# Optimization experiments

Measured on AMD Instinct MI355X. Metric: run time of the kernel, lower is better.

## Reference

```python
import jax, jax.numpy as jnp
import numpy as np

N_FEATURES = 16384
N_EXPERTS = 8
D_IN = 768
EXPERT_DIM = N_FEATURES // N_EXPERTS  # 2048
N_TOKENS = 16384


def setup_inputs() -> dict:
    key = jax.random.key(0)
    k_act, k_preb, k_enc, k_dec, k_rb, k_r = jax.random.split(key, 6)
    activations = jax.random.normal(k_act, (N_TOKENS, D_IN), dtype=jnp.float32)
    pre_b = jax.random.normal(k_preb, (D_IN,), dtype=jnp.float32) * 0.01
    enc = jax.random.normal(k_enc, (N_EXPERTS, D_IN, EXPERT_DIM), dtype=jnp.float32) / (2.0 ** 0.5) / (D_IN ** 0.5)
    dec = jax.random.normal(k_dec, (N_EXPERTS, EXPERT_DIM, D_IN), dtype=jnp.float32) / (EXPERT_DIM ** 0.5)
    router_b = jax.random.normal(k_rb, (D_IN,), dtype=jnp.float32) * 0.01
    router = jax.random.normal(k_r, (D_IN, N_EXPERTS), dtype=jnp.float32) / (D_IN ** 0.5)
    return {"activations": activations, "pre_b": pre_b, "enc": enc, "dec": dec,
            "router_b": router_b, "router": router}


def reference(activations, pre_b, enc, dec, router_b, router):
    # Router: softmax over experts, top-1 routing.
    logits = (activations - router_b) @ router            # [N, E]
    probs = jax.nn.softmax(logits, axis=-1)
    expert_max_prob = jnp.max(probs, axis=-1)              # [N]
    expert_idx = jnp.argmax(probs, axis=-1)                # [N] int

    n_experts = enc.shape[0]
    recons = jnp.zeros_like(activations)
    # Fixed small loop over experts; tokens are masked (zeroed) per expert so
    # each per-expert encode/decode GEMM only contributes for its routed rows.
    for e in range(n_experts):
        mask = (expert_idx == e)[:, None]                  # [N, 1]
        x_e = jnp.where(mask, activations, 0.0)            # masked gather
        latent = jax.nn.relu(x_e @ enc[e])                 # [N, expert_dim]
        recon = latent @ dec[e]                            # [N, d_in]
        recons = recons + jnp.where(mask, recon, 0.0)      # scatter-combine

    return expert_max_prob[:, None] * recons + pre_b
```

## Files before the change

kernel.cpp:

```cpp
#include <hip/hip_runtime.h>
#include <hip/hip_bf16.h>
#include <hip/hip_fp16.h>

#define N_TOKENS 16384
#define D_IN 768
#define N_EXPERTS 8
#define EXPERT_DIM 2048

#define ROUTER_BLOCKS 256
#define TOK_PER_BLOCK 64

typedef _Float16 half8 __attribute__((ext_vector_type(8)));
typedef float floatx4 __attribute__((ext_vector_type(4)));

#define BM 128
#define BN 128
#define BK 32

#define WAIT_VM4 0xF74
#define WAIT_VM0 0xF70

__device__ __forceinline__ void glds16(const _Float16* g, _Float16* l) {
    __builtin_amdgcn_global_load_lds(
        (const __attribute__((address_space(1))) unsigned int*)g,
        (__attribute__((address_space(3))) unsigned int*)l, 16, 0, 0);
}

__global__ __launch_bounds__(256) void convert_act(const float* __restrict__ act,
    _Float16* __restrict__ act_h)
{
    size_t i = ((size_t)blockIdx.x * 256 + threadIdx.x) * 8;
    float4 v0 = *(const float4*)(act + i);
    float4 v1 = *(const float4*)(act + i + 4);
    half8 h;
    h[0] = (_Float16)v0.x; h[1] = (_Float16)v0.y; h[2] = (_Float16)v0.z; h[3] = (_Float16)v0.w;
    h[4] = (_Float16)v1.x; h[5] = (_Float16)v1.y; h[6] = (_Float16)v1.z; h[7] = (_Float16)v1.w;
    *(half8*)(act_h + i) = h;
}

__global__ __launch_bounds__(256) void router_kernel(const float* __restrict__ act,
    const float* __restrict__ router_b, const float* __restrict__ router,
    float* __restrict__ prob, int* __restrict__ localpos, int* __restrict__ eidx,
    int* __restrict__ hist)
{
    __shared__ int h[N_EXPERTS];
    if (threadIdx.x < N_EXPERTS) h[threadIdx.x] = 0;
    __syncthreads();

    int wave = threadIdx.x >> 6, lane = threadIdx.x & 63;
#pragma unroll 1
    for (int it = 0; it < 16; ++it) {
        int t = blockIdx.x * TOK_PER_BLOCK + wave * 16 + it;
        float acc[8];
#pragma unroll
        for (int e = 0; e < 8; ++e) acc[e] = 0.f;
        const float* arow = act + (size_t)t * D_IN;
#pragma unroll
        for (int i0 = 0; i0 < D_IN; i0 += 64) {
            int i = i0 + lane;
            float a = arow[i] - router_b[i];
            const float* r = router + i * 8;
#pragma unroll
            for (int e = 0; e < 8; ++e) acc[e] += a * r[e];
        }
#pragma unroll
        for (int s = 32; s > 0; s >>= 1) {
#pragma unroll
            for (int e = 0; e < 8; ++e) acc[e] += __shfl_down(acc[e], s, 64);
        }
        if (lane == 0) {
            float m = acc[0]; int ai = 0;
#pragma unroll
            for (int e = 1; e < 8; ++e) if (acc[e] > m) { m = acc[e]; ai = e; }
            float s = 0.f;
#pragma unroll
            for (int e = 0; e < 8; ++e) s += __expf(acc[e] - m);
            prob[t] = 1.0f / s;
            eidx[t] = ai;
            localpos[t] = atomicAdd(&h[ai], 1);
        }
    }
    __syncthreads();
    if (threadIdx.x < N_EXPERTS) hist[blockIdx.x * N_EXPERTS + threadIdx.x] = h[threadIdx.x];
}

__global__ __launch_bounds__(256) void scan_kernel(int* __restrict__ hist,
    int* __restrict__ counts, int* __restrict__ offsets)
{
    __shared__ int sh[ROUTER_BLOCKS * N_EXPERTS];
    __shared__ int tot[N_EXPERTS], off[N_EXPERTS];
    int tid = threadIdx.x;
    *(int4*)&sh[tid * 8]     = *(const int4*)&hist[tid * 8];
    *(int4*)&sh[tid * 8 + 4] = *(const int4*)&hist[tid * 8 + 4];
    __syncthreads();
    if (tid < N_EXPERTS) {
        int run = 0;
        for (int b = 0; b < ROUTER_BLOCKS; ++b) {
            int v = sh[b * 8 + tid];
            sh[b * 8 + tid] = run;
            run += v;
        }
        tot[tid] = run;
    }
    __syncthreads();
    if (tid == 0) {
        int run = 0;
        for (int e = 0; e < N_EXPERTS; ++e) {
            off[e] = run; offsets[e] = run; counts[e] = tot[e]; run += tot[e];
        }
    }
    __syncthreads();
    int4 a = *(const int4*)&sh[tid * 8];
    int4 b = *(const int4*)&sh[tid * 8 + 4];
    a.x += off[0]; a.y += off[1]; a.z += off[2]; a.w += off[3];
    b.x += off[4]; b.y += off[5]; b.z += off[6]; b.w += off[7];
    *(int4*)&hist[tid * 8]     = a;
    *(int4*)&hist[tid * 8 + 4] = b;
}

__global__ __launch_bounds__(256) void order_kernel(const int* __restrict__ eidx,
    const int* __restrict__ localpos, const int* __restrict__ hist,
    int* __restrict__ order)
{
    int t = blockIdx.x * 256 + threadIdx.x;
    int base = hist[(t >> 6) * N_EXPERTS + eidx[t]];
    order[base + localpos[t]] = t;
}

__global__ __launch_bounds__(256) void transpose_to_half(const float* __restrict__ W,
    _Float16* __restrict__ WT, int K, int Nc)
{
    __shared__ _Float16 tile[64][72];
    size_t esz = (size_t)K * Nc;
    const float* We = W + (size_t)blockIdx.z * esz;
    _Float16* WTe = WT + (size_t)blockIdx.z * esz;
    int n0 = blockIdx.x * 64, k0 = blockIdx.y * 64;
    int tr = threadIdx.x >> 4;
    int tc = threadIdx.x & 15;
#pragma unroll
    for (int rr = 0; rr < 64; rr += 16) {
        int k = k0 + rr + tr;
        float4 v = *(const float4*)(We + (size_t)k * Nc + n0 + tc * 4);
        tile[tc * 4 + 0][rr + tr] = (_Float16)v.x;
        tile[tc * 4 + 1][rr + tr] = (_Float16)v.y;
        tile[tc * 4 + 2][rr + tr] = (_Float16)v.z;
        tile[tc * 4 + 3][rr + tr] = (_Float16)v.w;
    }
    __syncthreads();
#pragma unroll
    for (int p = 0; p < 2; ++p) {
        int id = threadIdx.x + p * 256;
        int r = id >> 3, ch = id & 7;
        half8 v = *(const half8*)&tile[r][ch * 8];
        *(half8*)(WTe + (size_t)(n0 + r) * K + k0 + ch * 8) = v;
    }
}

__global__ __launch_bounds__(256) void encode_kernel(const _Float16* __restrict__ act_h,
    const _Float16* __restrict__ encT, const int* __restrict__ order,
    const int* __restrict__ counts, const int* __restrict__ offsets,
    _Float16* __restrict__ latent)
{
    int e = blockIdx.z;
    int n_e = counts[e];
    int mt = blockIdx.y;
    if (mt * BM >= n_e) return;
    int nt = blockIdx.x;
    int slot0 = offsets[e] + mt * BM;
    int mrem = n_e - mt * BM;

    __shared__ _Float16 As[2][BM * BK];
    __shared__ _Float16 Bs[2][BN * BK];
    __shared__ int s_tok[BM];

    int tid = threadIdx.x;
    if (tid < BM) s_tok[tid] = (tid < mrem) ? order[slot0 + tid] : 0;
    __syncthreads();

    int wave = tid >> 6, lane = tid & 63;
    int wm = wave >> 1, wn = wave & 1;

    int r_lo = wave * 16 + (lane >> 2);
    int sc = lane & 3;
    int c = (sc - (r_lo >> 1)) & 3;
    const _Float16* Be = encT + (size_t)e * D_IN * EXPERT_DIM + (size_t)(nt * BN) * D_IN;
    const _Float16* pa0 = act_h + (size_t)s_tok[r_lo] * D_IN + c * 8;
    const _Float16* pa1 = act_h + (size_t)s_tok[r_lo + 64] * D_IN + c * 8;
    const _Float16* pb0 = Be + (size_t)r_lo * D_IN + c * 8;
    const _Float16* pb1 = Be + (size_t)(r_lo + 64) * D_IN + c * 8;

    int frag_off = ((((lane >> 4) + ((lane & 15) >> 1)) & 3) * 8);
    int mrow = lane & 15;

    floatx4 acc[4][4];
#pragma unroll
    for (int i = 0; i < 4; ++i)
#pragma unroll
        for (int j = 0; j < 4; ++j) acc[i][j] = (floatx4){0.f, 0.f, 0.f, 0.f};

#define ENC_ISSUE(kk, buf)                                            \
    do {                                                              \
        int k0_ = (kk) * BK;                                          \
        glds16(pa0 + k0_, &As[buf][(wave * 64) * 8]);                 \
        glds16(pa1 + k0_, &As[buf][(256 + wave * 64) * 8]);           \
        glds16(pb0 + k0_, &Bs[buf][(wave * 64) * 8]);                 \
        glds16(pb1 + k0_, &Bs[buf][(256 + wave * 64) * 8]);           \
    } while (0)

    const int NT = D_IN / BK;
    ENC_ISSUE(0, 0);
#pragma unroll 1
    for (int k = 0; k < NT; ++k) {
        if (k + 1 < NT) {
            ENC_ISSUE(k + 1, (k + 1) & 1);
            __builtin_amdgcn_s_waitcnt(WAIT_VM4);
        } else {
            __builtin_amdgcn_s_waitcnt(WAIT_VM0);
        }
        __builtin_amdgcn_s_barrier();
        int b = k & 1;
        half8 af[4], bf[4];
#pragma unroll
        for (int i = 0; i < 4; ++i) af[i] = *(const half8*)&As[b][(wm * 64 + i * 16 + mrow) * BK + frag_off];
#pragma unroll
        for (int i = 0; i < 4; ++i) bf[i] = *(const half8*)&Bs[b][(wn * 64 + i * 16 + mrow) * BK + frag_off];
#pragma unroll
        for (int i = 0; i < 4; ++i)
#pragma unroll
            for (int j = 0; j < 4; ++j)
                acc[i][j] = __builtin_amdgcn_mfma_f32_16x16x32_f16(af[i], bf[j], acc[i][j], 0, 0, 0);
        __builtin_amdgcn_s_barrier();
    }
#undef ENC_ISSUE

    int crow_base = wm * 64 + (lane >> 4) * 4;
    int ccol_base = nt * BN + wn * 64 + (lane & 15);
#pragma unroll
    for (int i = 0; i < 4; ++i) {
#pragma unroll
        for (int j = 0; j < 4; ++j) {
#pragma unroll
            for (int r = 0; r < 4; ++r) {
                int row = crow_base + i * 16 + r;
                if (row < mrem) {
                    float v = acc[i][j][r];
                    v = v > 0.f ? v : 0.f;
                    latent[(size_t)(slot0 + row) * EXPERT_DIM + ccol_base + j * 16] = (_Float16)v;
                }
            }
        }
    }
}

__global__ __launch_bounds__(256) void decode_kernel(const _Float16* __restrict__ latent,
    const _Float16* __restrict__ decT, const int* __restrict__ order,
    const int* __restrict__ counts, const int* __restrict__ offsets,
    const float* __restrict__ prob, const float* __restrict__ pre_b,
    float* __restrict__ out)
{
    int e = blockIdx.z;
    int n_e = counts[e];
    int mt = blockIdx.y;
    if (mt * BM >= n_e) return;
    int nt = blockIdx.x;
    int slot0 = offsets[e] + mt * BM;
    int mrem = n_e - mt * BM;

    __shared__ _Float16 As[2][BM * BK];
    __shared__ _Float16 Bs[2][BN * BK];
    __shared__ int s_tok[BM];
    __shared__ float s_p[BM];

    int tid = threadIdx.x;
    if (tid < BM) {
        int tok = (tid < mrem) ? order[slot0 + tid] : 0;
        s_tok[tid] = tok;
        s_p[tid] = prob[tok];
    }

    const _Float16* Ae = latent + (size_t)slot0 * EXPERT_DIM;
    const _Float16* Be = decT + (size_t)e * EXPERT_DIM * D_IN + (size_t)(nt * BN) * EXPERT_DIM;

    int wave = tid >> 6, lane = tid & 63;
    int wm = wave >> 1, wn = wave & 1;

    int r_lo = wave * 16 + (lane >> 2);
    int sc = lane & 3;
    int c = (sc - (r_lo >> 1)) & 3;
    const _Float16* pa0 = Ae + (size_t)r_lo * EXPERT_DIM + c * 8;
    const _Float16* pa1 = Ae + (size_t)(r_lo + 64) * EXPERT_DIM + c * 8;
    const _Float16* pb0 = Be + (size_t)r_lo * EXPERT_DIM + c * 8;
    const _Float16* pb1 = Be + (size_t)(r_lo + 64) * EXPERT_DIM + c * 8;

    int frag_off = ((((lane >> 4) + ((lane & 15) >> 1)) & 3) * 8);
    int mrow = lane & 15;

    floatx4 acc[4][4];
#pragma unroll
    for (int i = 0; i < 4; ++i)
#pragma unroll
        for (int j = 0; j < 4; ++j) acc[i][j] = (floatx4){0.f, 0.f, 0.f, 0.f};

#define DEC_ISSUE(kk, buf)                                            \
    do {                                                              \
        int k0_ = (kk) * BK;                                          \
        glds16(pa0 + k0_, &As[buf][(wave * 64) * 8]);                 \
        glds16(pa1 + k0_, &As[buf][(256 + wave * 64) * 8]);           \
        glds16(pb0 + k0_, &Bs[buf][(wave * 64) * 8]);                 \
        glds16(pb1 + k0_, &Bs[buf][(256 + wave * 64) * 8]);           \
    } while (0)

    const int NT = EXPERT_DIM / BK;
    DEC_ISSUE(0, 0);
#pragma unroll 1
    for (int k = 0; k < NT; ++k) {
        if (k + 1 < NT) {
            DEC_ISSUE(k + 1, (k + 1) & 1);
            __builtin_amdgcn_s_waitcnt(WAIT_VM4);
        } else {
            __builtin_amdgcn_s_waitcnt(WAIT_VM0);
        }
        __builtin_amdgcn_s_barrier();
        int b = k & 1;
        half8 af[4], bf[4];
#pragma unroll
        for (int i = 0; i < 4; ++i) af[i] = *(const half8*)&As[b][(wm * 64 + i * 16 + mrow) * BK + frag_off];
#pragma unroll
        for (int i = 0; i < 4; ++i) bf[i] = *(const half8*)&Bs[b][(wn * 64 + i * 16 + mrow) * BK + frag_off];
#pragma unroll
        for (int i = 0; i < 4; ++i)
#pragma unroll
            for (int j = 0; j < 4; ++j)
                acc[i][j] = __builtin_amdgcn_mfma_f32_16x16x32_f16(af[i], bf[j], acc[i][j], 0, 0, 0);
        __builtin_amdgcn_s_barrier();
    }
#undef DEC_ISSUE

    int crow_base = wm * 64 + (lane >> 4) * 4;
    int ccol_base = nt * BN + wn * 64 + (lane & 15);
#pragma unroll
    for (int i = 0; i < 4; ++i) {
#pragma unroll
        for (int j = 0; j < 4; ++j) {
            int col = ccol_base + j * 16;
            float pb = pre_b[col];
#pragma unroll
            for (int r = 0; r < 4; ++r) {
                int row = crow_base + i * 16 + r;
                if (row < mrem) {
                    out[(size_t)s_tok[row] * D_IN + col] = s_p[row] * acc[i][j][r] + pb;
                }
            }
        }
    }
}

extern "C" void kernel_launch(void* const* d_in, const int* in_sizes, int n_in,
                              void* d_out, int out_size, void* d_ws, size_t ws_size,
                              hipStream_t stream)
{
    const float* act      = (const float*)d_in[0];
    const float* pre_b    = (const float*)d_in[1];
    const float* enc      = (const float*)d_in[2];
    const float* dec      = (const float*)d_in[3];
    const float* router_b = (const float*)d_in[4];
    const float* router   = (const float*)d_in[5];
    float* out = (float*)d_out;

    char* w = (char*)d_ws;
    int* counts  = (int*)w;  w += 256;
    int* offsets = (int*)w;  w += 256;
    int* hist    = (int*)w;  w += ROUTER_BLOCKS * N_EXPERTS * 4;
    int* eidx    = (int*)w;  w += N_TOKENS * 4;
    int* lpos    = (int*)w;  w += N_TOKENS * 4;
    int* order   = (int*)w;  w += N_TOKENS * 4;
    float* prob  = (float*)w; w += N_TOKENS * 4;
    _Float16* act_h  = (_Float16*)w; w += (size_t)N_TOKENS * D_IN * 2;
    _Float16* encT   = (_Float16*)w; w += (size_t)N_EXPERTS * D_IN * EXPERT_DIM * 2;
    _Float16* decT   = (_Float16*)w; w += (size_t)N_EXPERTS * D_IN * EXPERT_DIM * 2;
    _Float16* latent = (_Float16*)w; w += (size_t)(N_TOKENS + BM) * EXPERT_DIM * 2;

    router_kernel<<<ROUTER_BLOCKS, 256, 0, stream>>>(act, router_b, router, prob, lpos, eidx, hist);
    scan_kernel<<<1, 256, 0, stream>>>(hist, counts, offsets);
    order_kernel<<<N_TOKENS / 256, 256, 0, stream>>>(eidx, lpos, hist, order);

    convert_act<<<N_TOKENS * D_IN / (256 * 8), 256, 0, stream>>>(act, act_h);
    transpose_to_half<<<dim3(EXPERT_DIM / 64, D_IN / 64, N_EXPERTS), 256, 0, stream>>>(enc, encT, D_IN, EXPERT_DIM);
    transpose_to_half<<<dim3(D_IN / 64, EXPERT_DIM / 64, N_EXPERTS), 256, 0, stream>>>(dec, decT, EXPERT_DIM, D_IN);

    encode_kernel<<<dim3(EXPERT_DIM / BN, N_TOKENS / BM, N_EXPERTS), 256, 0, stream>>>(
        act_h, encT, order, counts, offsets, latent);
    decode_kernel<<<dim3(D_IN / BN, N_TOKENS / BM, N_EXPERTS), 256, 0, stream>>>(
        latent, decT, order, counts, offsets, prob, pre_b, out);
}
```

Before: 407.9 us.

## Triple-buffer GEMM K-loop and remap block grid for expert-aware scheduling

Encode and decode GEMMs move from double to triple LDS buffering, prefetching two K-tiles ahead with a vmcnt-8 wait so global loads have more latency hiding. The 3D grid is replaced by a flat 1D grid whose index is decoded so groups of 8 consecutive blocks share the same M-tile across different (expert, N-tile) pairs, which changes the dispatch order and may improve L2 reuse of activation rows. A missing __syncthreads after the s_tok/s_p fill in decode is added. Extra LDS use (about 48KB per block) may reduce occupancy.

```diff
diff --git a/kernel.cpp b/kernel.cpp
--- a/kernel.cpp
+++ b/kernel.cpp
@@ -16,7 +16,9 @@
 #define BM 128
 #define BN 128
 #define BK 32
-
+#define NBUF 3
+
+#define WAIT_VM8 0xF78
 #define WAIT_VM4 0xF74
 #define WAIT_VM0 0xF70
 
@@ -161,16 +163,18 @@
     const int* __restrict__ counts, const int* __restrict__ offsets,
     _Float16* __restrict__ latent)
 {
-    int e = blockIdx.z;
+    int id = blockIdx.x;
+    int P = (id & 7) + 8 * ((id >> 3) >> 7);
+    int mt = (id >> 3) & 127;
+    int e = P >> 4, nt = P & 15;
+
     int n_e = counts[e];
-    int mt = blockIdx.y;
     if (mt * BM >= n_e) return;
-    int nt = blockIdx.x;
     int slot0 = offsets[e] + mt * BM;
     int mrem = n_e - mt * BM;
 
-    __shared__ _Float16 As[2][BM * BK];
-    __shared__ _Float16 Bs[2][BN * BK];
+    __shared__ _Float16 As[NBUF][BM * BK];
+    __shared__ _Float16 Bs[NBUF][BN * BK];
     __shared__ int s_tok[BM];
 
     int tid = threadIdx.x;
@@ -209,27 +213,32 @@
 
     const int NT = D_IN / BK;
     ENC_ISSUE(0, 0);
+    ENC_ISSUE(1, 1);
+    int buf = 0, nxt = 2;
 #pragma unroll 1
     for (int k = 0; k < NT; ++k) {
-        if (k + 1 < NT) {
-            ENC_ISSUE(k + 1, (k + 1) & 1);
+        if (k + 2 < NT) {
+            ENC_ISSUE(k + 2, nxt);
+            __builtin_amdgcn_s_waitcnt(WAIT_VM8);
+        } else if (k + 1 < NT) {
             __builtin_amdgcn_s_waitcnt(WAIT_VM4);
         } else {
             __builtin_amdgcn_s_waitcnt(WAIT_VM0);
         }
         __builtin_amdgcn_s_barrier();
-        int b = k & 1;
         half8 af[4], bf[4];
 #pragma unroll
-        for (int i = 0; i < 4; ++i) af[i] = *(const half8*)&As[b][(wm * 64 + i * 16 + mrow) * BK + frag_off];
-#pragma unroll
-        for (int i = 0; i < 4; ++i) bf[i] = *(const half8*)&Bs[b][(wn * 64 + i * 16 + mrow) * BK + frag_off];
+        for (int i = 0; i < 4; ++i) af[i] = *(const half8*)&As[buf][(wm * 64 + i * 16 + mrow) * BK + frag_off];
+#pragma unroll
+        for (int i = 0; i < 4; ++i) bf[i] = *(const half8*)&Bs[buf][(wn * 64 + i * 16 + mrow) * BK + frag_off];
 #pragma unroll
         for (int i = 0; i < 4; ++i)
 #pragma unroll
             for (int j = 0; j < 4; ++j)
                 acc[i][j] = __builtin_amdgcn_mfma_f32_16x16x32_f16(af[i], bf[j], acc[i][j], 0, 0, 0);
         __builtin_amdgcn_s_barrier();
+        buf = (buf == NBUF - 1) ? 0 : buf + 1;
+        nxt = (nxt == NBUF - 1) ? 0 : nxt + 1;
     }
 #undef ENC_ISSUE
 
@@ -258,16 +267,18 @@
     const float* __restrict__ prob, const float* __restrict__ pre_b,
     float* __restrict__ out)
 {
-    int e = blockIdx.z;
+    int id = blockIdx.x;
+    int P = (id & 7) + 8 * ((id >> 3) >> 7);
+    int mt = (id >> 3) & 127;
+    int e = P / 6, nt = P - e * 6;
+
     int n_e = counts[e];
-    int mt = blockIdx.y;
     if (mt * BM >= n_e) return;
-    int nt = blockIdx.x;
     int slot0 = offsets[e] + mt * BM;
     int mrem = n_e - mt * BM;
 
-    __shared__ _Float16 As[2][BM * BK];
-    __shared__ _Float16 Bs[2][BN * BK];
+    __shared__ _Float16 As[NBUF][BM * BK];
+    __shared__ _Float16 Bs[NBUF][BN * BK];
     __shared__ int s_tok[BM];
     __shared__ float s_p[BM];
 
@@ -277,6 +288,7 @@
         s_tok[tid] = tok;
         s_p[tid] = prob[tok];
     }
+    __syncthreads();
 
     const _Float16* Ae = latent + (size_t)slot0 * EXPERT_DIM;
     const _Float16* Be = decT + (size_t)e * EXPERT_DIM * D_IN + (size_t)(nt * BN) * EXPERT_DIM;
@@ -312,27 +324,32 @@
 
     const int NT = EXPERT_DIM / BK;
     DEC_ISSUE(0, 0);
+    DEC_ISSUE(1, 1);
+    int buf = 0, nxt = 2;
 #pragma unroll 1
     for (int k = 0; k < NT; ++k) {
-        if (k + 1 < NT) {
-            DEC_ISSUE(k + 1, (k + 1) & 1);
+        if (k + 2 < NT) {
+            DEC_ISSUE(k + 2, nxt);
+            __builtin_amdgcn_s_waitcnt(WAIT_VM8);
+        } else if (k + 1 < NT) {
             __builtin_amdgcn_s_waitcnt(WAIT_VM4);
         } else {
             __builtin_amdgcn_s_waitcnt(WAIT_VM0);
         }
         __builtin_amdgcn_s_barrier();
-        int b = k & 1;
         half8 af[4], bf[4];
 #pragma unroll
-        for (int i = 0; i < 4; ++i) af[i] = *(const half8*)&As[b][(wm * 64 + i * 16 + mrow) * BK + frag_off];
-#pragma unroll
-        for (int i = 0; i < 4; ++i) bf[i] = *(const half8*)&Bs[b][(wn * 64 + i * 16 + mrow) * BK + frag_off];
+        for (int i = 0; i < 4; ++i) af[i] = *(const half8*)&As[buf][(wm * 64 + i * 16 + mrow) * BK + frag_off];
+#pragma unroll
+        for (int i = 0; i < 4; ++i) bf[i] = *(const half8*)&Bs[buf][(wn * 64 + i * 16 + mrow) * BK + frag_off];
 #pragma unroll
         for (int i = 0; i < 4; ++i)
 #pragma unroll
             for (int j = 0; j < 4; ++j)
                 acc[i][j] = __builtin_amdgcn_mfma_f32_16x16x32_f16(af[i], bf[j], acc[i][j], 0, 0, 0);
         __builtin_amdgcn_s_barrier();
+        buf = (buf == NBUF - 1) ? 0 : buf + 1;
+        nxt = (nxt == NBUF - 1) ? 0 : nxt + 1;
     }
 #undef DEC_ISSUE
 
@@ -388,8 +405,6 @@
     transpose_to_half<<<dim3(EXPERT_DIM / 64, D_IN / 64, N_EXPERTS), 256, 0, stream>>>(enc, encT, D_IN, EXPERT_DIM);
     transpose_to_half<<<dim3(D_IN / 64, EXPERT_DIM / 64, N_EXPERTS), 256, 0, stream>>>(dec, decT, EXPERT_DIM, D_IN);
 
-    encode_kernel<<<dim3(EXPERT_DIM / BN, N_TOKENS / BM, N_EXPERTS), 256, 0, stream>>>(
-        act_h, encT, order, counts, offsets, latent);
-    decode_kernel<<<dim3(D_IN / BN, N_TOKENS / BM, N_EXPERTS), 256, 0, stream>>>(
-        latent, decT, order, counts, offsets, prob, pre_b, out);
-}
+    encode_kernel<<<16384, 256, 0, stream>>>(act_h, encT, order, counts, offsets, latent);
+    decode_kernel<<<6144, 256, 0, stream>>>(latent, decT, order, counts, offsets, prob, pre_b, out);
+}
```

Measured after the change: 403.8 us. Within noise of the previous version (-1.0%).
